# Kernel optimization log

Hardware: AMD Instinct MI355X
Metric: run time of the kernel (lower is better)

## Reference

```python
import jax, jax.numpy as jnp
import numpy as np
from jax import lax

EPS = 1e-5

def _rsign(x, beta):
    # per-channel learnable shift followed by sign binarization
    return jnp.sign(x + beta[None, :, None, None])

def _scaled_sign_conv(x, w, stride, pad):
    # XNOR-style binarized weights: sign(W) * mean(|W|) per output filter
    alpha = jnp.mean(jnp.abs(w), axis=(1, 2, 3), keepdims=True)
    wb = jnp.sign(w) * alpha
    return lax.conv_general_dilated(x, wb, (stride, stride), [(pad, pad), (pad, pad)],
                                    dimension_numbers=('NCHW', 'OIHW', 'NCHW'))

def _bn(x, gamma, beta):
    # training-mode batch norm (batch statistics), matching torch default forward
    m = jnp.mean(x, axis=(0, 2, 3), keepdims=True)
    v = jnp.var(x, axis=(0, 2, 3), keepdims=True)
    xn = (x - m) * lax.rsqrt(v + EPS)
    return xn * gamma[None, :, None, None] + beta[None, :, None, None]

def _rprelu(x, gamma, zeta, slope):
    g = gamma[None, :, None, None]
    s = slope[None, :, None, None]
    xs = x - g
    return jnp.where(xs > 0, xs, s * xs) + zeta[None, :, None, None]

def _avgpool2(x):
    B, C, H, W = x.shape
    return x.reshape(B, C, H // 2, 2, W // 2, 2).mean(axis=(3, 5))

def reference(x, rsign1_beta, w1, bn1_gamma, bn1_beta, rsign2_beta, w2, bn2_gamma, bn2_beta, pr_gamma, pr_zeta, pr_slope):
    # layer1: RSign -> 3x3 stride-2 scaled_sign conv -> BN
    out1 = _bn(_scaled_sign_conv(_rsign(x, rsign1_beta), w1, 2, 1), bn1_gamma, bn1_beta)
    out1 = out1 + _avgpool2(x)
    out1 = _rprelu(out1, pr_gamma, pr_zeta, pr_slope)
    # layer2 (shared weights, called twice with identical inputs -> identical outputs)
    out2 = _bn(_scaled_sign_conv(_rsign(out1, rsign2_beta), w2, 1, 0), bn2_gamma, bn2_beta)
    y = out2 + out1
    return jnp.concatenate([y, y], axis=1)

def setup_inputs() -> dict:
    key = jax.random.key(0)
    ks = jax.random.split(key, 8)
    B, C, H, W = 32, 256, 56, 56
    return {
        'x': jax.random.normal(ks[0], (B, C, H, W), jnp.float32),
        'rsign1_beta': jax.random.normal(ks[1], (C,), jnp.float32) * 0.1,
        'w1': jax.random.normal(ks[2], (C, C, 3, 3), jnp.float32) * 0.05,
        'bn1_gamma': jnp.ones((C,), jnp.float32),
        'bn1_beta': jnp.zeros((C,), jnp.float32),
        'rsign2_beta': jax.random.normal(ks[3], (C,), jnp.float32) * 0.1,
        'w2': jax.random.normal(ks[4], (C, C, 1, 1), jnp.float32) * 0.05,
        'bn2_gamma': jnp.ones((C,), jnp.float32),
        'bn2_beta': jnp.zeros((C,), jnp.float32),
        'pr_gamma': jax.random.normal(ks[5], (C,), jnp.float32) * 0.1,
        'pr_zeta': jax.random.normal(ks[6], (C,), jnp.float32) * 0.1,
        'pr_slope': jnp.full((C,), 0.25, jnp.float32),
    }
```

## Files before the change

kernel.cpp:

```cpp
#include <hip/hip_runtime.h>
#include <stdint.h>

typedef unsigned long long u64;
typedef uint32_t u32;

#define BB  32
#define CC  256
#define HH  56
#define WW  56
#define OHH 28
#define OWW 28
#define NPIX (BB*OHH*OWW)

__global__ __launch_bounds__(256) void rrb_prep_w(const float* __restrict__ w1,
                                                  const float* __restrict__ w2,
                                                  u32* __restrict__ wp1, u32* __restrict__ wp2,
                                                  float* __restrict__ alpha1, float* __restrict__ alpha2,
                                                  u32* __restrict__ stats_zero) {
    __shared__ float red[256];
    int co = blockIdx.x & 255;
    int t = threadIdx.x;
    int wid = t >> 6, lane = t & 63;
    if (blockIdx.x == 0) {
        #pragma unroll
        for (int k = 0; k < 6; ++k) stats_zero[k * 256 + t] = 0u;
    }
    float asum = 0.f;
    if (blockIdx.x < 256) {
        const float* wr = w1 + (size_t)co * 2304 + (size_t)t * 9;
        float v[9];
        #pragma unroll
        for (int k = 0; k < 9; ++k) { v[k] = wr[k]; asum += fabsf(v[k]); }
        #pragma unroll
        for (int k = 0; k < 9; ++k) {
            u64 m = __ballot(v[k] > 0.f);
            if (lane == 0)
                *(u64*)&wp1[((size_t)co * 9 + k) * 8 + 2 * wid] = m;
        }
    } else {
        float v = w2[co * 256 + t];
        asum = fabsf(v);
        u64 m = __ballot(v > 0.f);
        if (lane == 0) *(u64*)&wp2[co * 8 + 2 * wid] = m;
    }
    red[t] = asum; __syncthreads();
    for (int st = 128; st > 0; st >>= 1) {
        if (t < st) red[t] += red[t + st];
        __syncthreads();
    }
    if (t == 0) {
        if (blockIdx.x < 256) alpha1[co] = red[0] / 2304.f;
        else                  alpha2[co] = red[0] / 256.f;
    }
}

__global__ __launch_bounds__(256) void rrb_pack_x(const float* __restrict__ x,
                                                  const float* __restrict__ rsb1,
                                                  u32* __restrict__ xb, float* __restrict__ pool) {
    int i = blockIdx.x * 256 + threadIdx.x;
    int s  = i & 3;
    int i2 = i >> 2;
    int ow = i2 % OWW;
    int i3 = i2 / OWW;
    int oh = i3 % OHH;
    int i4 = i3 / OHH;
    int n  = i4 & 31;
    int j  = i4 >> 5;
    int c0 = 32 * j + 8 * s;
    const float* base = x + (((size_t)(n * CC + c0) * HH + 2 * oh) * WW + 2 * ow);

    float2 a0[8], a1[8];
    #pragma unroll
    for (int cc = 0; cc < 8; ++cc) {
        const float* p = base + (size_t)cc * (HH * WW);
        a0[cc] = *(const float2*)p;
        a1[cc] = *(const float2*)(p + WW);
    }
    float4 b0 = *(const float4*)&rsb1[c0];
    float4 b1 = *(const float4*)&rsb1[c0 + 4];

    u32 w00 = 0, w01 = 0, w10 = 0, w11 = 0;
    float pv[8];
    #pragma unroll
    for (int cc = 0; cc < 8; ++cc) {
        float b = (cc < 4) ? ((const float*)&b0)[cc] : ((const float*)&b1)[cc - 4];
        w00 |= (u32)(a0[cc].x + b > 0.f) << cc;
        w01 |= (u32)(a0[cc].y + b > 0.f) << cc;
        w10 |= (u32)(a1[cc].x + b > 0.f) << cc;
        w11 |= (u32)(a1[cc].y + b > 0.f) << cc;
        pv[cc] = (a0[cc].x + a0[cc].y + a1[cc].x + a1[cc].y) * 0.25f;
    }
    w00 <<= 8 * s; w01 <<= 8 * s; w10 <<= 8 * s; w11 <<= 8 * s;
    w00 |= __shfl_xor(w00, 1); w00 |= __shfl_xor(w00, 2);
    w01 |= __shfl_xor(w01, 1); w01 |= __shfl_xor(w01, 2);
    w10 |= __shfl_xor(w10, 1); w10 |= __shfl_xor(w10, 2);
    w11 |= __shfl_xor(w11, 1); w11 |= __shfl_xor(w11, 2);

    float* pp = pool + ((size_t)(n * OHH + oh) * OWW + ow) * CC + c0;
    *(float4*)&pp[0] = make_float4(pv[0], pv[1], pv[2], pv[3]);
    *(float4*)&pp[4] = make_float4(pv[4], pv[5], pv[6], pv[7]);

    u32* xo = xb + (((size_t)(n * HH + 2 * oh) * WW + 2 * ow) * 8) + j;
    u32 wsel = (s == 0) ? w00 : (s == 1) ? w01 : (s == 2) ? w10 : w11;
    int off = (s == 0) ? 0 : (s == 1) ? 8 : (s == 2) ? WW * 8 : WW * 8 + 8;
    xo[off] = wsel;
}

__global__ __launch_bounds__(256) void rrb_conv1(const u32* __restrict__ xb,
                                                 const u32* __restrict__ wp1,
                                                 short* __restrict__ S1,
                                                 int* __restrict__ s_sum, u64* __restrict__ s_sq) {
    __shared__ u32 xs[3 * WW * 8];
    int blk = blockIdx.x;
    int n = blk / OHH, oh = blk - n * OHH;
    int t = threadIdx.x;
    int r0 = 2 * oh - 1;
    for (int i = t; i < 3 * WW * 8; i += 256) {
        int row = i / (WW * 8);
        int ih = r0 + row;
        xs[i] = (ih >= 0) ? xb[((size_t)(n * HH + ih) * WW) * 8 + (i - row * WW * 8)] : 0u;
    }
    u32 wreg[72];
    {
        const u32* wsrc = wp1 + (size_t)t * 72;
        #pragma unroll
        for (int i = 0; i < 72; ++i) wreg[i] = wsrc[i];
    }
    __syncthreads();
    bool oh0 = (oh == 0);
    int bsum = 0; long long bsq = 0;
    short* outp = S1 + ((size_t)(n * OHH + oh) * OWW) * CC + t;
    for (int ow = 0; ow < OWW; ++ow) {
        int S = 0;
        #pragma unroll
        for (int kh = 0; kh < 3; ++kh) {
            bool vkh = !(kh == 0 && oh0);
            #pragma unroll
            for (int kw = 0; kw < 3; ++kw) {
                int iw = 2 * ow + kw - 1;
                bool ok = vkh && (iw >= 0);
                int iwc = iw < 0 ? 0 : iw;
                const u32* xp = &xs[(kh * WW + iwc) * 8];
                int p = 0;
                #pragma unroll
                for (int j = 0; j < 8; ++j) p += __popc(xp[j] ^ wreg[(kh * 3 + kw) * 8 + j]);
                S += ok ? (256 - 2 * p) : 0;
            }
        }
        outp[ow * CC] = (short)S;
        bsum += S;
        bsq += (long long)S * S;
    }
    atomicAdd(&s_sum[t], bsum);
    atomicAdd(&s_sq[t], (u64)bsq);
}

__device__ __forceinline__ void bn_fold(const int* ssum, const u64* ssq,
                                        const float* alpha, const float* gamma,
                                        const float* beta, int c, float& a, float& b) {
    const double N = (double)NPIX;
    double s = (double)ssum[c];
    double q = (double)ssq[c];
    double mS = s / N;
    double vS = q / N - mS * mS;
    double al = (double)alpha[c];
    double scale = (double)gamma[c] / sqrt(al * al * vS + 1e-5);
    a = (float)(al * scale);
    b = (float)((double)beta[c] - al * mS * scale);
}

__global__ __launch_bounds__(256) void rrb_out1c2(const short* __restrict__ S1,
                                                  float* __restrict__ pool,
                                                  const int* __restrict__ ssum, const u64* __restrict__ ssq,
                                                  const float* __restrict__ alpha1,
                                                  const float* __restrict__ bn1g, const float* __restrict__ bn1b,
                                                  const float* __restrict__ pg, const float* __restrict__ pz,
                                                  const float* __restrict__ ps, const float* __restrict__ rsb2,
                                                  const u32* __restrict__ wp2,
                                                  int* __restrict__ s_sum2, u64* __restrict__ s_sq2) {
    __shared__ u32 xs[14 * 8];
    int blk = blockIdx.x;
    int half = blk & 1;
    int rest = blk >> 1;
    int n = rest / OHH, oh = rest - n * OHH;
    int owlo = half * 14;
    int c = threadIdx.x;
    int wid = c >> 6, lane = c & 63;
    float a, b;
    bn_fold(ssum, ssq, alpha1, bn1g, bn1b, c, a, b);
    float g = pg[c], z = pz[c], s = ps[c], b2 = rsb2[c];
    size_t pixbase = ((size_t)(n * OHH + oh) * OWW + owlo);
    const short* sp = S1 + pixbase * CC + c;
    float* pp = pool + pixbase * CC + c;
    float sv[14], pv[14];
    #pragma unroll
    for (int k = 0; k < 14; ++k) sv[k] = (float)sp[k * CC];
    #pragma unroll
    for (int k = 0; k < 14; ++k) pv[k] = pp[k * CC];
    #pragma unroll
    for (int k = 0; k < 14; ++k) {
        float v = a * sv[k] + b + pv[k];
        float xsv = v - g;
        float o = (xsv > 0.f ? xsv : s * xsv) + z;
        pp[k * CC] = o;
        u64 m = __ballot(o + b2 > 0.f);
        if (lane == 0) *(u64*)&xs[k * 8 + 2 * wid] = m;
    }
    __syncthreads();
    u32 wr[8];
    {
        const u32* wsv = wp2 + (size_t)c * 8;
        #pragma unroll
        for (int j = 0; j < 8; ++j) wr[j] = wsv[j];
    }
    int bsum = 0; long long bsq = 0;
    #pragma unroll
    for (int k = 0; k < 14; ++k) {
        int p = 0;
        #pragma unroll
        for (int j = 0; j < 8; ++j) p += __popc(xs[k * 8 + j] ^ wr[j]);
        int S = 256 - 2 * p;
        bsum += S;
        bsq += (long long)S * S;
    }
    atomicAdd(&s_sum2[c], bsum);
    atomicAdd(&s_sq2[c], (u64)bsq);
}

__global__ __launch_bounds__(256) void rrb_final(const float* __restrict__ out1,
                                                 const int* __restrict__ ssum, const u64* __restrict__ ssq,
                                                 const float* __restrict__ alpha2,
                                                 const float* __restrict__ bn2g, const float* __restrict__ bn2b,
                                                 const float* __restrict__ rsb2,
                                                 const u32* __restrict__ wp2,
                                                 float* __restrict__ y) {
    __shared__ u32 xs[OWW * 8];
    __shared__ float lds[256 * 29];
    int blk = blockIdx.x;
    int n = blk / OHH, oh = blk - n * OHH;
    int c = threadIdx.x;
    int wid = c >> 6, lane = c & 63;
    float a, b;
    bn_fold(ssum, ssq, alpha2, bn2g, bn2b, c, a, b);
    float b2 = rsb2[c];
    size_t pixbase = ((size_t)(n * OHH + oh) * OWW);
    const float* op = out1 + pixbase * CC + c;
    float ov[OWW];
    #pragma unroll
    for (int ow = 0; ow < OWW; ++ow) ov[ow] = op[ow * CC];
    #pragma unroll
    for (int ow = 0; ow < OWW; ++ow) {
        u64 m = __ballot(ov[ow] + b2 > 0.f);
        if (lane == 0) *(u64*)&xs[ow * 8 + 2 * wid] = m;
    }
    u32 wr[8];
    {
        const u32* wsv = wp2 + (size_t)c * 8;
        #pragma unroll
        for (int j = 0; j < 8; ++j) wr[j] = wsv[j];
    }
    __syncthreads();
    #pragma unroll
    for (int ow = 0; ow < OWW; ++ow) {
        int p = 0;
        #pragma unroll
        for (int j = 0; j < 8; ++j) p += __popc(xs[ow * 8 + j] ^ wr[j]);
        int S = 256 - 2 * p;
        lds[c * 29 + ow] = a * (float)S + b + ov[ow];
    }
    __syncthreads();
    #pragma unroll
    for (int it = 0; it < 7; ++it) {
        int idx = it * 256 + c;
        int cp = idx / 7, qq = idx - cp * 7;
        const float* lp = &lds[cp * 29 + 4 * qq];
        float4 v = make_float4(lp[0], lp[1], lp[2], lp[3]);
        float* dst = y + ((size_t)(n * 2 * CC + cp) * OHH + oh) * OWW + 4 * qq;
        *(float4*)dst = v;
        *(float4*)(dst + (size_t)CC * OHH * OWW) = v;
    }
}

extern "C" void kernel_launch(void* const* d_in, const int* in_sizes, int n_in,
                              void* d_out, int out_size, void* d_ws, size_t ws_size,
                              hipStream_t stream) {
    const float* x    = (const float*)d_in[0];
    const float* rsb1 = (const float*)d_in[1];
    const float* w1   = (const float*)d_in[2];
    const float* bn1g = (const float*)d_in[3];
    const float* bn1b = (const float*)d_in[4];
    const float* rsb2 = (const float*)d_in[5];
    const float* w2   = (const float*)d_in[6];
    const float* bn2g = (const float*)d_in[7];
    const float* bn2b = (const float*)d_in[8];
    const float* pg   = (const float*)d_in[9];
    const float* pz   = (const float*)d_in[10];
    const float* ps   = (const float*)d_in[11];
    float* y = (float*)d_out;

    char* ws = (char*)d_ws;
    if (ws_size < 41840640) return;

    u32*   wp1    = (u32*)(ws + 0);
    u32*   wp2    = (u32*)(ws + 73728);
    float* alpha1 = (float*)(ws + 81920);
    float* alpha2 = (float*)(ws + 82944);
    int*   st1_sum = (int*)(ws + 88064);
    u64*   st1_sq  = (u64*)(ws + 89088);
    int*   st2_sum = (int*)(ws + 91136);
    u64*   st2_sq  = (u64*)(ws + 92160);
    u32*   xb   = (u32*)(ws + 94208);
    float* pool = (float*)(ws + 3305472);
    short* S1   = (short*)(ws + 28995584);

    rrb_prep_w<<<512, 256, 0, stream>>>(w1, w2, wp1, wp2, alpha1, alpha2,
                                        (u32*)(ws + 88064));
    rrb_pack_x<<<(BB * OHH * OWW * 8 * 4) / 256, 256, 0, stream>>>(x, rsb1, xb, pool);
    rrb_conv1<<<BB * OHH, 256, 0, stream>>>(xb, wp1, S1, st1_sum, st1_sq);
    rrb_out1c2<<<BB * OHH * 2, 256, 0, stream>>>(S1, pool, st1_sum, st1_sq, alpha1,
                                                 bn1g, bn1b, pg, pz, ps, rsb2,
                                                 wp2, st2_sum, st2_sq);
    rrb_final<<<BB * OHH, 256, 0, stream>>>(pool, st2_sum, st2_sq, alpha2,
                                            bn2g, bn2b, rsb2, wp2, y);
}
```

Baseline: 149.6 us.

## Fuse conv1, out1/conv2 stats, and final into persistent kernel with grid barriers

```diff
diff --git a/kernel.cpp b/kernel.cpp
--- a/kernel.cpp
+++ b/kernel.cpp
@@ -11,52 +11,57 @@
 #define OHH 28
 #define OWW 28
 #define NPIX (BB*OHH*OWW)
-
-__global__ __launch_bounds__(256) void rrb_prep_w(const float* __restrict__ w1,
-                                                  const float* __restrict__ w2,
-                                                  u32* __restrict__ wp1, u32* __restrict__ wp2,
-                                                  float* __restrict__ alpha1, float* __restrict__ alpha2,
-                                                  u32* __restrict__ stats_zero) {
-    __shared__ float red[256];
-    int co = blockIdx.x & 255;
-    int t = threadIdx.x;
-    int wid = t >> 6, lane = t & 63;
-    if (blockIdx.x == 0) {
-        #pragma unroll
-        for (int k = 0; k < 6; ++k) stats_zero[k * 256 + t] = 0u;
-    }
-    float asum = 0.f;
-    if (blockIdx.x < 256) {
-        const float* wr = w1 + (size_t)co * 2304 + (size_t)t * 9;
-        float v[9];
-        #pragma unroll
-        for (int k = 0; k < 9; ++k) { v[k] = wr[k]; asum += fabsf(v[k]); }
-        #pragma unroll
-        for (int k = 0; k < 9; ++k) {
-            u64 m = __ballot(v[k] > 0.f);
-            if (lane == 0)
-                *(u64*)&wp1[((size_t)co * 9 + k) * 8 + 2 * wid] = m;
-        }
-    } else {
-        float v = w2[co * 256 + t];
-        asum = fabsf(v);
-        u64 m = __ballot(v > 0.f);
-        if (lane == 0) *(u64*)&wp2[co * 8 + 2 * wid] = m;
-    }
-    red[t] = asum; __syncthreads();
-    for (int st = 128; st > 0; st >>= 1) {
-        if (t < st) red[t] += red[t + st];
-        __syncthreads();
-    }
-    if (t == 0) {
-        if (blockIdx.x < 256) alpha1[co] = red[0] / 2304.f;
-        else                  alpha2[co] = red[0] / 256.f;
-    }
-}
-
-__global__ __launch_bounds__(256) void rrb_pack_x(const float* __restrict__ x,
-                                                  const float* __restrict__ rsb1,
-                                                  u32* __restrict__ xb, float* __restrict__ pool) {
+#define PACKBLKS 3136
+#define FGRID (BB*OHH)
+
+__global__ __launch_bounds__(256) void rrb_prep_pack(const float* __restrict__ x,
+                                                     const float* __restrict__ rsb1,
+                                                     const float* __restrict__ w1,
+                                                     const float* __restrict__ w2,
+                                                     u32* __restrict__ xb, float* __restrict__ pool,
+                                                     u32* __restrict__ wp1, u32* __restrict__ wp2,
+                                                     float* __restrict__ alpha1, float* __restrict__ alpha2,
+                                                     u32* __restrict__ stats_zero, int* __restrict__ bar) {
+    if (blockIdx.x >= PACKBLKS) {
+        __shared__ float red[256];
+        int pb = blockIdx.x - PACKBLKS;
+        int co = pb & 255;
+        int t = threadIdx.x;
+        int wid = t >> 6, lane = t & 63;
+        if (pb == 0) {
+            #pragma unroll
+            for (int k = 0; k < 6; ++k) stats_zero[k * 256 + t] = 0u;
+            if (t == 0) *bar = 0;
+        }
+        float asum = 0.f;
+        if (pb < 256) {
+            const float* wr = w1 + (size_t)co * 2304 + (size_t)t * 9;
+            float v[9];
+            #pragma unroll
+            for (int k = 0; k < 9; ++k) { v[k] = wr[k]; asum += fabsf(v[k]); }
+            #pragma unroll
+            for (int k = 0; k < 9; ++k) {
+                u64 m = __ballot(v[k] > 0.f);
+                if (lane == 0)
+                    *(u64*)&wp1[((size_t)co * 9 + k) * 8 + 2 * wid] = m;
+            }
+        } else {
+            float v = w2[co * 256 + t];
+            asum = fabsf(v);
+            u64 m = __ballot(v > 0.f);
+            if (lane == 0) *(u64*)&wp2[co * 8 + 2 * wid] = m;
+        }
+        red[t] = asum; __syncthreads();
+        for (int st = 128; st > 0; st >>= 1) {
+            if (t < st) red[t] += red[t + st];
+            __syncthreads();
+        }
+        if (t == 0) {
+            if (pb < 256) alpha1[co] = red[0] / 2304.f;
+            else          alpha2[co] = red[0] / 256.f;
+        }
+        return;
+    }
     int i = blockIdx.x * 256 + threadIdx.x;
     int s  = i & 3;
     int i2 = i >> 2;
@@ -106,178 +111,164 @@
     xo[off] = wsel;
 }
 
-__global__ __launch_bounds__(256) void rrb_conv1(const u32* __restrict__ xb,
-                                                 const u32* __restrict__ wp1,
-                                                 short* __restrict__ S1,
-                                                 int* __restrict__ s_sum, u64* __restrict__ s_sq) {
-    __shared__ u32 xs[3 * WW * 8];
-    int blk = blockIdx.x;
-    int n = blk / OHH, oh = blk - n * OHH;
-    int t = threadIdx.x;
-    int r0 = 2 * oh - 1;
-    for (int i = t; i < 3 * WW * 8; i += 256) {
-        int row = i / (WW * 8);
-        int ih = r0 + row;
-        xs[i] = (ih >= 0) ? xb[((size_t)(n * HH + ih) * WW) * 8 + (i - row * WW * 8)] : 0u;
-    }
-    u32 wreg[72];
-    {
-        const u32* wsrc = wp1 + (size_t)t * 72;
-        #pragma unroll
-        for (int i = 0; i < 72; ++i) wreg[i] = wsrc[i];
-    }
+__device__ __forceinline__ void gbar(int* cnt, int target) {
     __syncthreads();
-    bool oh0 = (oh == 0);
-    int bsum = 0; long long bsq = 0;
-    short* outp = S1 + ((size_t)(n * OHH + oh) * OWW) * CC + t;
-    for (int ow = 0; ow < OWW; ++ow) {
-        int S = 0;
-        #pragma unroll
-        for (int kh = 0; kh < 3; ++kh) {
-            bool vkh = !(kh == 0 && oh0);
-            #pragma unroll
-            for (int kw = 0; kw < 3; ++kw) {
-                int iw = 2 * ow + kw - 1;
-                bool ok = vkh && (iw >= 0);
-                int iwc = iw < 0 ? 0 : iw;
-                const u32* xp = &xs[(kh * WW + iwc) * 8];
-                int p = 0;
-                #pragma unroll
-                for (int j = 0; j < 8; ++j) p += __popc(xp[j] ^ wreg[(kh * 3 + kw) * 8 + j]);
-                S += ok ? (256 - 2 * p) : 0;
-            }
-        }
-        outp[ow * CC] = (short)S;
-        bsum += S;
-        bsq += (long long)S * S;
-    }
-    atomicAdd(&s_sum[t], bsum);
-    atomicAdd(&s_sq[t], (u64)bsq);
-}
-
-__device__ __forceinline__ void bn_fold(const int* ssum, const u64* ssq,
-                                        const float* alpha, const float* gamma,
-                                        const float* beta, int c, float& a, float& b) {
+    if (threadIdx.x == 0) {
+        __threadfence();
+        __hip_atomic_fetch_add(cnt, 1, __ATOMIC_ACQ_REL, __HIP_MEMORY_SCOPE_AGENT);
+        int guard = 0;
+        while (__hip_atomic_load(cnt, __ATOMIC_ACQUIRE, __HIP_MEMORY_SCOPE_AGENT) < target) {
+            __builtin_amdgcn_s_sleep(8);
+            if (++guard > (1 << 22)) break;
+        }
+    }
+    __syncthreads();
+}
+
+__device__ __forceinline__ void bn_fold_v(int sv, u64 qv, float al_, float g_, float be_,
+                                          float& a, float& b) {
     const double N = (double)NPIX;
-    double s = (double)ssum[c];
-    double q = (double)ssq[c];
+    double s = (double)sv;
+    double q = (double)qv;
     double mS = s / N;
     double vS = q / N - mS * mS;
-    double al = (double)alpha[c];
-    double scale = (double)gamma[c] / sqrt(al * al * vS + 1e-5);
+    double al = (double)al_;
+    double scale = (double)g_ / sqrt(al * al * vS + 1e-5);
     a = (float)(al * scale);
-    b = (float)((double)beta[c] - al * mS * scale);
-}
-
-__global__ __launch_bounds__(256) void rrb_out1c2(const short* __restrict__ S1,
-                                                  float* __restrict__ pool,
-                                                  const int* __restrict__ ssum, const u64* __restrict__ ssq,
-                                                  const float* __restrict__ alpha1,
-                                                  const float* __restrict__ bn1g, const float* __restrict__ bn1b,
-                                                  const float* __restrict__ pg, const float* __restrict__ pz,
-                                                  const float* __restrict__ ps, const float* __restrict__ rsb2,
-                                                  const u32* __restrict__ wp2,
-                                                  int* __restrict__ s_sum2, u64* __restrict__ s_sq2) {
-    __shared__ u32 xs[14 * 8];
-    int blk = blockIdx.x;
-    int half = blk & 1;
-    int rest = blk >> 1;
-    int n = rest / OHH, oh = rest - n * OHH;
-    int owlo = half * 14;
-    int c = threadIdx.x;
-    int wid = c >> 6, lane = c & 63;
-    float a, b;
-    bn_fold(ssum, ssq, alpha1, bn1g, bn1b, c, a, b);
-    float g = pg[c], z = pz[c], s = ps[c], b2 = rsb2[c];
-    size_t pixbase = ((size_t)(n * OHH + oh) * OWW + owlo);
-    const short* sp = S1 + pixbase * CC + c;
-    float* pp = pool + pixbase * CC + c;
-    float sv[14], pv[14];
-    #pragma unroll
-    for (int k = 0; k < 14; ++k) sv[k] = (float)sp[k * CC];
-    #pragma unroll
-    for (int k = 0; k < 14; ++k) pv[k] = pp[k * CC];
-    #pragma unroll
-    for (int k = 0; k < 14; ++k) {
-        float v = a * sv[k] + b + pv[k];
-        float xsv = v - g;
-        float o = (xsv > 0.f ? xsv : s * xsv) + z;
-        pp[k * CC] = o;
-        u64 m = __ballot(o + b2 > 0.f);
-        if (lane == 0) *(u64*)&xs[k * 8 + 2 * wid] = m;
-    }
-    __syncthreads();
-    u32 wr[8];
-    {
-        const u32* wsv = wp2 + (size_t)c * 8;
-        #pragma unroll
-        for (int j = 0; j < 8; ++j) wr[j] = wsv[j];
-    }
-    int bsum = 0; long long bsq = 0;
-    #pragma unroll
-    for (int k = 0; k < 14; ++k) {
-        int p = 0;
-        #pragma unroll
-        for (int j = 0; j < 8; ++j) p += __popc(xs[k * 8 + j] ^ wr[j]);
-        int S = 256 - 2 * p;
-        bsum += S;
-        bsq += (long long)S * S;
-    }
-    atomicAdd(&s_sum2[c], bsum);
-    atomicAdd(&s_sq2[c], (u64)bsq);
-}
-
-__global__ __launch_bounds__(256) void rrb_final(const float* __restrict__ out1,
-                                                 const int* __restrict__ ssum, const u64* __restrict__ ssq,
-                                                 const float* __restrict__ alpha2,
-                                                 const float* __restrict__ bn2g, const float* __restrict__ bn2b,
-                                                 const float* __restrict__ rsb2,
-                                                 const u32* __restrict__ wp2,
-                                                 float* __restrict__ y) {
-    __shared__ u32 xs[OWW * 8];
-    __shared__ float lds[256 * 29];
+    b = (float)((double)be_ - al * mS * scale);
+}
+
+__global__ __launch_bounds__(256, 4) void rrb_fused(const u32* __restrict__ xb,
+                                                    const u32* __restrict__ wp1,
+                                                    const u32* __restrict__ wp2,
+                                                    const float* __restrict__ pool,
+                                                    int* __restrict__ st1_sum, u64* __restrict__ st1_sq,
+                                                    int* __restrict__ st2_sum, u64* __restrict__ st2_sq,
+                                                    const float* __restrict__ alpha1,
+                                                    const float* __restrict__ bn1g, const float* __restrict__ bn1b,
+                                                    const float* __restrict__ alpha2,
+                                                    const float* __restrict__ bn2g, const float* __restrict__ bn2b,
+                                                    const float* __restrict__ pg, const float* __restrict__ pz,
+                                                    const float* __restrict__ ps, const float* __restrict__ rsb2,
+                                                    float* __restrict__ y, int* __restrict__ bar) {
+    __shared__ char shraw[256 * 29 * 4 + OWW * 8 * 4];
+    u32*   xs   = (u32*)shraw;
+    float* tb   = (float*)shraw;
+    u32*   bits = (u32*)(shraw + 256 * 29 * 4);
+
     int blk = blockIdx.x;
     int n = blk / OHH, oh = blk - n * OHH;
     int c = threadIdx.x;
     int wid = c >> 6, lane = c & 63;
-    float a, b;
-    bn_fold(ssum, ssq, alpha2, bn2g, bn2b, c, a, b);
-    float b2 = rsb2[c];
-    size_t pixbase = ((size_t)(n * OHH + oh) * OWW);
-    const float* op = out1 + pixbase * CC + c;
+
+    int r0 = 2 * oh - 1;
+    for (int i = c; i < 3 * WW * 8; i += 256) {
+        int row = i / (WW * 8);
+        int ih = r0 + row;
+        xs[i] = (ih >= 0) ? xb[((size_t)(n * HH + ih) * WW) * 8 + (i - row * WW * 8)] : 0u;
+    }
+    u32 svp[14];
+    {
+        u32 wreg[72];
+        const u32* wsrc = wp1 + (size_t)c * 72;
+        #pragma unroll
+        for (int i = 0; i < 72; ++i) wreg[i] = wsrc[i];
+        __syncthreads();
+        bool oh0 = (oh == 0);
+        int bsum = 0; long long bsq = 0;
+        #pragma unroll
+        for (int ow = 0; ow < OWW; ++ow) {
+            int S = 0;
+            #pragma unroll
+            for (int kh = 0; kh < 3; ++kh) {
+                bool vkh = !(kh == 0 && oh0);
+                #pragma unroll
+                for (int kw = 0; kw < 3; ++kw) {
+                    int iw = 2 * ow + kw - 1;
+                    bool ok = vkh && (iw >= 0);
+                    int iwc = iw < 0 ? 0 : iw;
+                    const u32* xp = &xs[(kh * WW + iwc) * 8];
+                    int p = 0;
+                    #pragma unroll
+                    for (int j = 0; j < 8; ++j) p += __popc(xp[j] ^ wreg[(kh * 3 + kw) * 8 + j]);
+                    S += ok ? (256 - 2 * p) : 0;
+                }
+            }
+            if ((ow & 1) == 0) svp[ow >> 1] = (u32)(S & 0xffff);
+            else               svp[ow >> 1] |= (u32)(S & 0xffff) << 16;
+            bsum += S;
+            bsq += (long long)S * S;
+        }
+        atomicAdd(&st1_sum[c], bsum);
+        atomicAdd(&st1_sq[c], (u64)bsq);
+    }
+
+    gbar(bar, FGRID);
+
     float ov[OWW];
-    #pragma unroll
-    for (int ow = 0; ow < OWW; ++ow) ov[ow] = op[ow * CC];
-    #pragma unroll
-    for (int ow = 0; ow < OWW; ++ow) {
-        u64 m = __ballot(ov[ow] + b2 > 0.f);
-        if (lane == 0) *(u64*)&xs[ow * 8 + 2 * wid] = m;
-    }
-    u32 wr[8];
+    u32 wr2[8];
     {
+        int s1v = __hip_atomic_load(&st1_sum[c], __ATOMIC_RELAXED, __HIP_MEMORY_SCOPE_AGENT);
+        u64 q1v = __hip_atomic_load(&st1_sq[c], __ATOMIC_RELAXED, __HIP_MEMORY_SCOPE_AGENT);
+        float a1, b1;
+        bn_fold_v(s1v, q1v, alpha1[c], bn1g[c], bn1b[c], a1, b1);
+        float g = pg[c], z = pz[c], sl = ps[c], b2 = rsb2[c];
+        const float* pp = pool + ((size_t)(n * OHH + oh) * OWW) * CC + c;
+        #pragma unroll
+        for (int k = 0; k < OWW; ++k) {
+            int S = (k & 1) ? (((int)svp[k >> 1]) >> 16)
+                            : (((int)(svp[k >> 1] << 16)) >> 16);
+            float v = a1 * (float)S + b1 + pp[k * CC];
+            float xsv = v - g;
+            float o = (xsv > 0.f ? xsv : sl * xsv) + z;
+            ov[k] = o;
+            u64 m = __ballot(o + b2 > 0.f);
+            if (lane == 0) *(u64*)&bits[k * 8 + 2 * wid] = m;
+        }
         const u32* wsv = wp2 + (size_t)c * 8;
         #pragma unroll
-        for (int j = 0; j < 8; ++j) wr[j] = wsv[j];
-    }
-    __syncthreads();
-    #pragma unroll
-    for (int ow = 0; ow < OWW; ++ow) {
-        int p = 0;
-        #pragma unroll
-        for (int j = 0; j < 8; ++j) p += __popc(xs[ow * 8 + j] ^ wr[j]);
-        int S = 256 - 2 * p;
-        lds[c * 29 + ow] = a * (float)S + b + ov[ow];
-    }
-    __syncthreads();
-    #pragma unroll
-    for (int it = 0; it < 7; ++it) {
-        int idx = it * 256 + c;
-        int cp = idx / 7, qq = idx - cp * 7;
-        const float* lp = &lds[cp * 29 + 4 * qq];
-        float4 v = make_float4(lp[0], lp[1], lp[2], lp[3]);
-        float* dst = y + ((size_t)(n * 2 * CC + cp) * OHH + oh) * OWW + 4 * qq;
-        *(float4*)dst = v;
-        *(float4*)(dst + (size_t)CC * OHH * OWW) = v;
+        for (int j = 0; j < 8; ++j) wr2[j] = wsv[j];
+        __syncthreads();
+        int bsum = 0; long long bsq = 0;
+        #pragma unroll
+        for (int k = 0; k < OWW; ++k) {
+            int p = 0;
+            #pragma unroll
+            for (int j = 0; j < 8; ++j) p += __popc(bits[k * 8 + j] ^ wr2[j]);
+            int S = 256 - 2 * p;
+            bsum += S;
+            bsq += (long long)S * S;
+        }
+        atomicAdd(&st2_sum[c], bsum);
+        atomicAdd(&st2_sq[c], (u64)bsq);
+    }
+
+    gbar(bar, 2 * FGRID);
+
+    {
+        int s2v = __hip_atomic_load(&st2_sum[c], __ATOMIC_RELAXED, __HIP_MEMORY_SCOPE_AGENT);
+        u64 q2v = __hip_atomic_load(&st2_sq[c], __ATOMIC_RELAXED, __HIP_MEMORY_SCOPE_AGENT);
+        float a2, b2f;
+        bn_fold_v(s2v, q2v, alpha2[c], bn2g[c], bn2b[c], a2, b2f);
+        #pragma unroll
+        for (int ow = 0; ow < OWW; ++ow) {
+            int p = 0;
+            #pragma unroll
+            for (int j = 0; j < 8; ++j) p += __popc(bits[ow * 8 + j] ^ wr2[j]);
+            int S = 256 - 2 * p;
+            tb[c * 29 + ow] = a2 * (float)S + b2f + ov[ow];
+        }
+        __syncthreads();
+        #pragma unroll
+        for (int it = 0; it < 7; ++it) {
+            int idx = it * 256 + c;
+            int cp = idx / 7, qq = idx - cp * 7;
+            const float* lp = &tb[cp * 29 + 4 * qq];
+            float4 v = make_float4(lp[0], lp[1], lp[2], lp[3]);
+            float* dst = y + ((size_t)(n * 2 * CC + cp) * OHH + oh) * OWW + 4 * qq;
+            *(float4*)dst = v;
+            *(float4*)(dst + (size_t)CC * OHH * OWW) = v;
+        }
     }
 }
 
@@ -299,27 +290,27 @@
     float* y = (float*)d_out;
 
     char* ws = (char*)d_ws;
-    if (ws_size < 41840640) return;
+    if (ws_size < 28995584) return;
 
     u32*   wp1    = (u32*)(ws + 0);
     u32*   wp2    = (u32*)(ws + 73728);
     float* alpha1 = (float*)(ws + 81920);
     float* alpha2 = (float*)(ws + 82944);
+    int*   bar     = (int*)(ws + 84992);
     int*   st1_sum = (int*)(ws + 88064);
     u64*   st1_sq  = (u64*)(ws + 89088);
     int*   st2_sum = (int*)(ws + 91136);
     u64*   st2_sq  = (u64*)(ws + 92160);
     u32*   xb   = (u32*)(ws + 94208);
     float* pool = (float*)(ws + 3305472);
-    short* S1   = (short*)(ws + 28995584);
-
-    rrb_prep_w<<<512, 256, 0, stream>>>(w1, w2, wp1, wp2, alpha1, alpha2,
-                                        (u32*)(ws + 88064));
-    rrb_pack_x<<<(BB * OHH * OWW * 8 * 4) / 256, 256, 0, stream>>>(x, rsb1, xb, pool);
-    rrb_conv1<<<BB * OHH, 256, 0, stream>>>(xb, wp1, S1, st1_sum, st1_sq);
-    rrb_out1c2<<<BB * OHH * 2, 256, 0, stream>>>(S1, pool, st1_sum, st1_sq, alpha1,
-                                                 bn1g, bn1b, pg, pz, ps, rsb2,
-                                                 wp2, st2_sum, st2_sq);
-    rrb_final<<<BB * OHH, 256, 0, stream>>>(pool, st2_sum, st2_sq, alpha2,
-                                            bn2g, bn2b, rsb2, wp2, y);
-}
+
+    u32* stats_zero = (u32*)(ws + 88064);
+
+    rrb_prep_pack<<<PACKBLKS + 512, 256, 0, stream>>>(x, rsb1, w1, w2, xb, pool,
+                                                      wp1, wp2, alpha1, alpha2,
+                                                      stats_zero, bar);
+    rrb_fused<<<FGRID, 256, 0, stream>>>(xb, wp1, wp2, pool,
+                                         st1_sum, st1_sq, st2_sum, st2_sq,
+                                         alpha1, bn1g, bn1b, alpha2, bn2g, bn2b,
+                                         pg, pz, ps, rsb2, y, bar);
+}
```

After: 242.0 us. +61.8%, slower.

## Replace BN-stat atomics with per-block partials and dedicated reduce kernels; fuse weight prep

Applied to the files above, without the earlier changes.

```diff
diff --git a/kernel.cpp b/kernel.cpp
--- a/kernel.cpp
+++ b/kernel.cpp
@@ -11,52 +11,50 @@
 #define OHH 28
 #define OWW 28
 #define NPIX (BB*OHH*OWW)
-
-__global__ __launch_bounds__(256) void rrb_prep_w(const float* __restrict__ w1,
-                                                  const float* __restrict__ w2,
-                                                  u32* __restrict__ wp1, u32* __restrict__ wp2,
-                                                  float* __restrict__ alpha1, float* __restrict__ alpha2,
-                                                  u32* __restrict__ stats_zero) {
-    __shared__ float red[256];
-    int co = blockIdx.x & 255;
-    int t = threadIdx.x;
-    int wid = t >> 6, lane = t & 63;
-    if (blockIdx.x == 0) {
-        #pragma unroll
-        for (int k = 0; k < 6; ++k) stats_zero[k * 256 + t] = 0u;
-    }
-    float asum = 0.f;
-    if (blockIdx.x < 256) {
-        const float* wr = w1 + (size_t)co * 2304 + (size_t)t * 9;
-        float v[9];
-        #pragma unroll
-        for (int k = 0; k < 9; ++k) { v[k] = wr[k]; asum += fabsf(v[k]); }
-        #pragma unroll
-        for (int k = 0; k < 9; ++k) {
-            u64 m = __ballot(v[k] > 0.f);
-            if (lane == 0)
-                *(u64*)&wp1[((size_t)co * 9 + k) * 8 + 2 * wid] = m;
+#define PACKBLKS 3136
+
+__global__ __launch_bounds__(256) void rrb_prep_pack(const float* __restrict__ x,
+                                                     const float* __restrict__ rsb1,
+                                                     const float* __restrict__ w1,
+                                                     const float* __restrict__ w2,
+                                                     u32* __restrict__ xb, float* __restrict__ pool,
+                                                     u32* __restrict__ wp1, u32* __restrict__ wp2,
+                                                     float* __restrict__ alpha1, float* __restrict__ alpha2) {
+    if (blockIdx.x >= PACKBLKS) {
+        __shared__ float red[256];
+        int pb = blockIdx.x - PACKBLKS;
+        int co = pb & 255;
+        int t = threadIdx.x;
+        int wid = t >> 6, lane = t & 63;
+        float asum = 0.f;
+        if (pb < 256) {
+            const float* wr = w1 + (size_t)co * 2304 + (size_t)t * 9;
+            float v[9];
+            #pragma unroll
+            for (int k = 0; k < 9; ++k) { v[k] = wr[k]; asum += fabsf(v[k]); }
+            #pragma unroll
+            for (int k = 0; k < 9; ++k) {
+                u64 m = __ballot(v[k] > 0.f);
+                if (lane == 0)
+                    *(u64*)&wp1[((size_t)co * 9 + k) * 8 + 2 * wid] = m;
+            }
+        } else {
+            float v = w2[co * 256 + t];
+            asum = fabsf(v);
+            u64 m = __ballot(v > 0.f);
+            if (lane == 0) *(u64*)&wp2[co * 8 + 2 * wid] = m;
         }
-    } else {
-        float v = w2[co * 256 + t];
-        asum = fabsf(v);
-        u64 m = __ballot(v > 0.f);
-        if (lane == 0) *(u64*)&wp2[co * 8 + 2 * wid] = m;
-    }
-    red[t] = asum; __syncthreads();
-    for (int st = 128; st > 0; st >>= 1) {
-        if (t < st) red[t] += red[t + st];
-        __syncthreads();
-    }
-    if (t == 0) {
-        if (blockIdx.x < 256) alpha1[co] = red[0] / 2304.f;
-        else                  alpha2[co] = red[0] / 256.f;
-    }
-}
-
-__global__ __launch_bounds__(256) void rrb_pack_x(const float* __restrict__ x,
-                                                  const float* __restrict__ rsb1,
-                                                  u32* __restrict__ xb, float* __restrict__ pool) {
+        red[t] = asum; __syncthreads();
+        for (int st = 128; st > 0; st >>= 1) {
+            if (t < st) red[t] += red[t + st];
+            __syncthreads();
+        }
+        if (t == 0) {
+            if (pb < 256) alpha1[co] = red[0] / 2304.f;
+            else          alpha2[co] = red[0] / 256.f;
+        }
+        return;
+    }
     int i = blockIdx.x * 256 + threadIdx.x;
     int s  = i & 3;
     int i2 = i >> 2;
@@ -109,7 +107,7 @@
 __global__ __launch_bounds__(256) void rrb_conv1(const u32* __restrict__ xb,
                                                  const u32* __restrict__ wp1,
                                                  short* __restrict__ S1,
-                                                 int* __restrict__ s_sum, u64* __restrict__ s_sq) {
+                                                 int* __restrict__ P1s, int* __restrict__ P1q) {
     __shared__ u32 xs[3 * WW * 8];
     int blk = blockIdx.x;
     int n = blk / OHH, oh = blk - n * OHH;
@@ -128,7 +126,7 @@
     }
     __syncthreads();
     bool oh0 = (oh == 0);
-    int bsum = 0; long long bsq = 0;
+    int bsum = 0, bsq = 0;
     short* outp = S1 + ((size_t)(n * OHH + oh) * OWW) * CC + t;
     for (int ow = 0; ow < OWW; ++ow) {
         int S = 0;
@@ -149,36 +147,54 @@
         }
         outp[ow * CC] = (short)S;
         bsum += S;
-        bsq += (long long)S * S;
-    }
-    atomicAdd(&s_sum[t], bsum);
-    atomicAdd(&s_sq[t], (u64)bsq);
-}
-
-__device__ __forceinline__ void bn_fold(const int* ssum, const u64* ssq,
-                                        const float* alpha, const float* gamma,
-                                        const float* beta, int c, float& a, float& b) {
-    const double N = (double)NPIX;
-    double s = (double)ssum[c];
-    double q = (double)ssq[c];
-    double mS = s / N;
-    double vS = q / N - mS * mS;
-    double al = (double)alpha[c];
-    double scale = (double)gamma[c] / sqrt(al * al * vS + 1e-5);
-    a = (float)(al * scale);
-    b = (float)((double)beta[c] - al * mS * scale);
+        bsq += S * S;
+    }
+    P1s[blk * CC + t] = bsum;
+    P1q[blk * CC + t] = bsq;
+}
+
+__global__ __launch_bounds__(256) void rrb_reduce(const int* __restrict__ Ps,
+                                                  const int* __restrict__ Pq,
+                                                  int nrows,
+                                                  const float* __restrict__ alpha,
+                                                  const float* __restrict__ gamma,
+                                                  const float* __restrict__ beta,
+                                                  float* __restrict__ A, float* __restrict__ Bv) {
+    __shared__ int rS[256], rQ[256];
+    int t = threadIdx.x;
+    int ks = t >> 5, co = t & 31;
+    int ch = blockIdx.x * 32 + co;
+    int aS = 0, aQ = 0;
+    for (int i = ks; i < nrows; i += 8) {
+        aS += Ps[i * CC + ch];
+        aQ += Pq[i * CC + ch];
+    }
+    rS[t] = aS; rQ[t] = aQ; __syncthreads();
+    if (t < 128) { rS[t] += rS[t + 128]; rQ[t] += rQ[t + 128]; } __syncthreads();
+    if (t < 64)  { rS[t] += rS[t + 64];  rQ[t] += rQ[t + 64];  } __syncthreads();
+    if (t < 32)  {
+        int sS = rS[t] + rS[t + 32];
+        int sQ = rQ[t] + rQ[t + 32];
+        const double N = (double)NPIX;
+        double s = (double)sS;
+        double q = (double)sQ;
+        double mS = s / N;
+        double vS = q / N - mS * mS;
+        double al = (double)alpha[ch];
+        double scale = (double)gamma[ch] / sqrt(al * al * vS + 1e-5);
+        A[ch]  = (float)(al * scale);
+        Bv[ch] = (float)((double)beta[ch] - al * mS * scale);
+    }
 }
 
 __global__ __launch_bounds__(256) void rrb_out1c2(const short* __restrict__ S1,
                                                   float* __restrict__ pool,
-                                                  const int* __restrict__ ssum, const u64* __restrict__ ssq,
-                                                  const float* __restrict__ alpha1,
-                                                  const float* __restrict__ bn1g, const float* __restrict__ bn1b,
+                                                  const float* __restrict__ A1, const float* __restrict__ B1,
                                                   const float* __restrict__ pg, const float* __restrict__ pz,
                                                   const float* __restrict__ ps, const float* __restrict__ rsb2,
                                                   const u32* __restrict__ wp2,
-                                                  int* __restrict__ s_sum2, u64* __restrict__ s_sq2) {
-    __shared__ u32 xs[14 * 8];
+                                                  int* __restrict__ P2s, int* __restrict__ P2q) {
+    __shared__ u32 bits[14 * 8];
     int blk = blockIdx.x;
     int half = blk & 1;
     int rest = blk >> 1;
@@ -186,8 +202,7 @@
     int owlo = half * 14;
     int c = threadIdx.x;
     int wid = c >> 6, lane = c & 63;
-    float a, b;
-    bn_fold(ssum, ssq, alpha1, bn1g, bn1b, c, a, b);
+    float a = A1[c], b = B1[c];
     float g = pg[c], z = pz[c], s = ps[c], b2 = rsb2[c];
     size_t pixbase = ((size_t)(n * OHH + oh) * OWW + owlo);
     const short* sp = S1 + pixbase * CC + c;
@@ -204,44 +219,41 @@
         float o = (xsv > 0.f ? xsv : s * xsv) + z;
         pp[k * CC] = o;
         u64 m = __ballot(o + b2 > 0.f);
-        if (lane == 0) *(u64*)&xs[k * 8 + 2 * wid] = m;
-    }
-    __syncthreads();
+        if (lane == 0) *(u64*)&bits[k * 8 + 2 * wid] = m;
+    }
     u32 wr[8];
     {
         const u32* wsv = wp2 + (size_t)c * 8;
         #pragma unroll
         for (int j = 0; j < 8; ++j) wr[j] = wsv[j];
     }
-    int bsum = 0; long long bsq = 0;
+    __syncthreads();
+    int bsum = 0, bsq = 0;
     #pragma unroll
     for (int k = 0; k < 14; ++k) {
         int p = 0;
         #pragma unroll
-        for (int j = 0; j < 8; ++j) p += __popc(xs[k * 8 + j] ^ wr[j]);
+        for (int j = 0; j < 8; ++j) p += __popc(bits[k * 8 + j] ^ wr[j]);
         int S = 256 - 2 * p;
         bsum += S;
-        bsq += (long long)S * S;
-    }
-    atomicAdd(&s_sum2[c], bsum);
-    atomicAdd(&s_sq2[c], (u64)bsq);
+        bsq += S * S;
+    }
+    P2s[blk * CC + c] = bsum;
+    P2q[blk * CC + c] = bsq;
 }
 
 __global__ __launch_bounds__(256) void rrb_final(const float* __restrict__ out1,
-                                                 const int* __restrict__ ssum, const u64* __restrict__ ssq,
-                                                 const float* __restrict__ alpha2,
-                                                 const float* __restrict__ bn2g, const float* __restrict__ bn2b,
+                                                 const float* __restrict__ A2, const float* __restrict__ B2,
                                                  const float* __restrict__ rsb2,
                                                  const u32* __restrict__ wp2,
                                                  float* __restrict__ y) {
-    __shared__ u32 xs[OWW * 8];
+    __shared__ u32 bits[OWW * 8];
     __shared__ float lds[256 * 29];
     int blk = blockIdx.x;
     int n = blk / OHH, oh = blk - n * OHH;
     int c = threadIdx.x;
     int wid = c >> 6, lane = c & 63;
-    float a, b;
-    bn_fold(ssum, ssq, alpha2, bn2g, bn2b, c, a, b);
+    float a = A2[c], b = B2[c];
     float b2 = rsb2[c];
     size_t pixbase = ((size_t)(n * OHH + oh) * OWW);
     const float* op = out1 + pixbase * CC + c;
@@ -251,7 +263,7 @@
     #pragma unroll
     for (int ow = 0; ow < OWW; ++ow) {
         u64 m = __ballot(ov[ow] + b2 > 0.f);
-        if (lane == 0) *(u64*)&xs[ow * 8 + 2 * wid] = m;
+        if (lane == 0) *(u64*)&bits[ow * 8 + 2 * wid] = m;
     }
     u32 wr[8];
     {
@@ -264,7 +276,7 @@
     for (int ow = 0; ow < OWW; ++ow) {
         int p = 0;
         #pragma unroll
-        for (int j = 0; j < 8; ++j) p += __popc(xs[ow * 8 + j] ^ wr[j]);
+        for (int j = 0; j < 8; ++j) p += __popc(bits[ow * 8 + j] ^ wr[j]);
         int S = 256 - 2 * p;
         lds[c * 29 + ow] = a * (float)S + b + ov[ow];
     }
@@ -299,27 +311,30 @@
     float* y = (float*)d_out;
 
     char* ws = (char*)d_ws;
-    if (ws_size < 41840640) return;
+    if (ws_size < 47345664) return;
 
     u32*   wp1    = (u32*)(ws + 0);
     u32*   wp2    = (u32*)(ws + 73728);
     float* alpha1 = (float*)(ws + 81920);
     float* alpha2 = (float*)(ws + 82944);
-    int*   st1_sum = (int*)(ws + 88064);
-    u64*   st1_sq  = (u64*)(ws + 89088);
-    int*   st2_sum = (int*)(ws + 91136);
-    u64*   st2_sq  = (u64*)(ws + 92160);
+    float* A1     = (float*)(ws + 83968);
+    float* B1     = (float*)(ws + 84992);
+    float* A2     = (float*)(ws + 86016);
+    float* B2     = (float*)(ws + 87040);
     u32*   xb   = (u32*)(ws + 94208);
     float* pool = (float*)(ws + 3305472);
     short* S1   = (short*)(ws + 28995584);
-
-    rrb_prep_w<<<512, 256, 0, stream>>>(w1, w2, wp1, wp2, alpha1, alpha2,
-                                        (u32*)(ws + 88064));
-    rrb_pack_x<<<(BB * OHH * OWW * 8 * 4) / 256, 256, 0, stream>>>(x, rsb1, xb, pool);
-    rrb_conv1<<<BB * OHH, 256, 0, stream>>>(xb, wp1, S1, st1_sum, st1_sq);
-    rrb_out1c2<<<BB * OHH * 2, 256, 0, stream>>>(S1, pool, st1_sum, st1_sq, alpha1,
-                                                 bn1g, bn1b, pg, pz, ps, rsb2,
-                                                 wp2, st2_sum, st2_sq);
-    rrb_final<<<BB * OHH, 256, 0, stream>>>(pool, st2_sum, st2_sq, alpha2,
-                                            bn2g, bn2b, rsb2, wp2, y);
-}
+    int*   P1s  = (int*)(ws + 41840640);
+    int*   P1q  = (int*)(ws + 42758144);
+    int*   P2s  = (int*)(ws + 43675648);
+    int*   P2q  = (int*)(ws + 45510656);
+
+    rrb_prep_pack<<<PACKBLKS + 512, 256, 0, stream>>>(x, rsb1, w1, w2, xb, pool,
+                                                      wp1, wp2, alpha1, alpha2);
+    rrb_conv1<<<BB * OHH, 256, 0, stream>>>(xb, wp1, S1, P1s, P1q);
+    rrb_reduce<<<8, 256, 0, stream>>>(P1s, P1q, BB * OHH, alpha1, bn1g, bn1b, A1, B1);
+    rrb_out1c2<<<BB * OHH * 2, 256, 0, stream>>>(S1, pool, A1, B1, pg, pz, ps, rsb2,
+                                                 wp2, P2s, P2q);
+    rrb_reduce<<<8, 256, 0, stream>>>(P2s, P2q, BB * OHH * 2, alpha2, bn2g, bn2b, A2, B2);
+    rrb_final<<<BB * OHH, 256, 0, stream>>>(pool, A2, B2, rsb2, wp2, y);
+}
```

Measured after the change: 205.3 us. 1.37x slower.

## Split conv1 input-channel reduction across two thread halves with LDS combine

Applied to the files above, without the earlier changes.

```diff
diff --git a/kernel.cpp b/kernel.cpp
--- a/kernel.cpp
+++ b/kernel.cpp
@@ -106,32 +106,39 @@
     xo[off] = wsel;
 }
 
-__global__ __launch_bounds__(256) void rrb_conv1(const u32* __restrict__ xb,
+__global__ __launch_bounds__(512) void rrb_conv1(const u32* __restrict__ xb,
                                                  const u32* __restrict__ wp1,
                                                  short* __restrict__ S1,
                                                  int* __restrict__ s_sum, u64* __restrict__ s_sq) {
     __shared__ u32 xs[3 * WW * 8];
+    __shared__ ushort qh[OWW][2][256];
     int blk = blockIdx.x;
     int n = blk / OHH, oh = blk - n * OHH;
     int t = threadIdx.x;
+    int c = t & 255;
+    int h = t >> 8;
     int r0 = 2 * oh - 1;
-    for (int i = t; i < 3 * WW * 8; i += 256) {
+    for (int i = t; i < 3 * WW * 8; i += 512) {
         int row = i / (WW * 8);
         int ih = r0 + row;
         xs[i] = (ih >= 0) ? xb[((size_t)(n * HH + ih) * WW) * 8 + (i - row * WW * 8)] : 0u;
     }
-    u32 wreg[72];
+    u32 wreg[36];
     {
-        const u32* wsrc = wp1 + (size_t)t * 72;
-        #pragma unroll
-        for (int i = 0; i < 72; ++i) wreg[i] = wsrc[i];
+        const u32* wsrc = wp1 + (size_t)c * 72 + 4 * h;
+        #pragma unroll
+        for (int k = 0; k < 9; ++k) {
+            wreg[4 * k + 0] = wsrc[8 * k + 0];
+            wreg[4 * k + 1] = wsrc[8 * k + 1];
+            wreg[4 * k + 2] = wsrc[8 * k + 2];
+            wreg[4 * k + 3] = wsrc[8 * k + 3];
+        }
     }
     __syncthreads();
     bool oh0 = (oh == 0);
-    int bsum = 0; long long bsq = 0;
-    short* outp = S1 + ((size_t)(n * OHH + oh) * OWW) * CC + t;
+    #pragma unroll
     for (int ow = 0; ow < OWW; ++ow) {
-        int S = 0;
+        int Q = 0;
         #pragma unroll
         for (int kh = 0; kh < 3; ++kh) {
             bool vkh = !(kh == 0 && oh0);
@@ -140,19 +147,31 @@
                 int iw = 2 * ow + kw - 1;
                 bool ok = vkh && (iw >= 0);
                 int iwc = iw < 0 ? 0 : iw;
-                const u32* xp = &xs[(kh * WW + iwc) * 8];
+                const u32* xp = &xs[(kh * WW + iwc) * 8 + 4 * h];
                 int p = 0;
                 #pragma unroll
-                for (int j = 0; j < 8; ++j) p += __popc(xp[j] ^ wreg[(kh * 3 + kw) * 8 + j]);
-                S += ok ? (256 - 2 * p) : 0;
+                for (int j = 0; j < 4; ++j) p += __popc(xp[j] ^ wreg[(kh * 3 + kw) * 4 + j]);
+                Q += ok ? p : 0;
             }
         }
-        outp[ow * CC] = (short)S;
-        bsum += S;
-        bsq += (long long)S * S;
-    }
-    atomicAdd(&s_sum[t], bsum);
-    atomicAdd(&s_sq[t], (u64)bsq);
+        qh[ow][h][c] = (ushort)Q;
+    }
+    __syncthreads();
+    if (h == 0) {
+        int rv = oh0 ? 2 : 3;
+        int bsum = 0; long long bsq = 0;
+        short* outp = S1 + ((size_t)(n * OHH + oh) * OWW) * CC + c;
+        #pragma unroll
+        for (int ow = 0; ow < OWW; ++ow) {
+            int V = rv * (ow == 0 ? 2 : 3);
+            int S = 256 * V - 2 * ((int)qh[ow][0][c] + (int)qh[ow][1][c]);
+            outp[ow * CC] = (short)S;
+            bsum += S;
+            bsq += (long long)S * S;
+        }
+        atomicAdd(&s_sum[c], bsum);
+        atomicAdd(&s_sq[c], (u64)bsq);
+    }
 }
 
 __device__ __forceinline__ void bn_fold(const int* ssum, const u64* ssq,
@@ -178,7 +197,7 @@
                                                   const float* __restrict__ ps, const float* __restrict__ rsb2,
                                                   const u32* __restrict__ wp2,
                                                   int* __restrict__ s_sum2, u64* __restrict__ s_sq2) {
-    __shared__ u32 xs[14 * 8];
+    __shared__ u32 xsb[14 * 8];
     int blk = blockIdx.x;
     int half = blk & 1;
     int rest = blk >> 1;
@@ -204,7 +223,7 @@
         float o = (xsv > 0.f ? xsv : s * xsv) + z;
         pp[k * CC] = o;
         u64 m = __ballot(o + b2 > 0.f);
-        if (lane == 0) *(u64*)&xs[k * 8 + 2 * wid] = m;
+        if (lane == 0) *(u64*)&xsb[k * 8 + 2 * wid] = m;
     }
     __syncthreads();
     u32 wr[8];
@@ -218,7 +237,7 @@
     for (int k = 0; k < 14; ++k) {
         int p = 0;
         #pragma unroll
-        for (int j = 0; j < 8; ++j) p += __popc(xs[k * 8 + j] ^ wr[j]);
+        for (int j = 0; j < 8; ++j) p += __popc(xsb[k * 8 + j] ^ wr[j]);
         int S = 256 - 2 * p;
         bsum += S;
         bsq += (long long)S * S;
@@ -234,7 +253,7 @@
                                                  const float* __restrict__ rsb2,
                                                  const u32* __restrict__ wp2,
                                                  float* __restrict__ y) {
-    __shared__ u32 xs[OWW * 8];
+    __shared__ u32 bits[OWW * 8];
     __shared__ float lds[256 * 29];
     int blk = blockIdx.x;
     int n = blk / OHH, oh = blk - n * OHH;
@@ -251,7 +270,7 @@
     #pragma unroll
     for (int ow = 0; ow < OWW; ++ow) {
         u64 m = __ballot(ov[ow] + b2 > 0.f);
-        if (lane == 0) *(u64*)&xs[ow * 8 + 2 * wid] = m;
+        if (lane == 0) *(u64*)&bits[ow * 8 + 2 * wid] = m;
     }
     u32 wr[8];
     {
@@ -264,7 +283,7 @@
     for (int ow = 0; ow < OWW; ++ow) {
         int p = 0;
         #pragma unroll
-        for (int j = 0; j < 8; ++j) p += __popc(xs[ow * 8 + j] ^ wr[j]);
+        for (int j = 0; j < 8; ++j) p += __popc(bits[ow * 8 + j] ^ wr[j]);
         int S = 256 - 2 * p;
         lds[c * 29 + ow] = a * (float)S + b + ov[ow];
     }
@@ -316,7 +335,7 @@
     rrb_prep_w<<<512, 256, 0, stream>>>(w1, w2, wp1, wp2, alpha1, alpha2,
                                         (u32*)(ws + 88064));
     rrb_pack_x<<<(BB * OHH * OWW * 8 * 4) / 256, 256, 0, stream>>>(x, rsb1, xb, pool);
-    rrb_conv1<<<BB * OHH, 256, 0, stream>>>(xb, wp1, S1, st1_sum, st1_sq);
+    rrb_conv1<<<BB * OHH, 512, 0, stream>>>(xb, wp1, S1, st1_sum, st1_sq);
     rrb_out1c2<<<BB * OHH * 2, 256, 0, stream>>>(S1, pool, st1_sum, st1_sq, alpha1,
                                                  bn1g, bn1b, pg, pz, ps, rsb2,
                                                  wp2, st2_sum, st2_sq);
```

Measured after the change: 147.8 us. Within noise of the previous version (-1.2%).
